# Kernel tuning notes

Measured on AMD Instinct MI355X. Metric: run time of the kernel, lower is better.

The kernel has to match this reference:

```python
import jax, jax.numpy as jnp
import numpy as np

N_NODES = 50000
N_EDGES = 800000
IN_CH = 128
OUT_CH = 64  # hidden = 2*OUT_CH = 128


def setup_inputs() -> dict:
    key = jax.random.key(0)
    ks = jax.random.split(key, 5)
    x = jax.random.normal(ks[0], (N_NODES, IN_CH), dtype=jnp.float32)
    edge_index = jax.random.randint(ks[1], (2, N_EDGES), 0, N_NODES, dtype=jnp.int32)
    # Glorot-ish scaled weights for the two GCNConv layers
    W1 = jax.random.normal(ks[2], (IN_CH, 2 * OUT_CH), dtype=jnp.float32) * 0.05
    b1 = jnp.zeros((2 * OUT_CH,), dtype=jnp.float32)
    W2 = jax.random.normal(ks[3], (2 * OUT_CH, OUT_CH), dtype=jnp.float32) * 0.05
    b2 = jnp.zeros((OUT_CH,), dtype=jnp.float32)
    return {"x": x, "edge_index": edge_index, "W1": W1, "b1": b1, "W2": W2, "b2": b2}


def reference(x, edge_index, W1, b1, W2, b2):
    N = x.shape[0]
    # GCN normalization with self-loops (PyG GCNConv default):
    # A_hat = A + I, deg from target nodes, norm = d_i^-1/2 * d_j^-1/2
    loops = jnp.arange(N, dtype=edge_index.dtype)
    row = jnp.concatenate([edge_index[0], loops])  # source
    col = jnp.concatenate([edge_index[1], loops])  # target
    deg = jax.ops.segment_sum(jnp.ones(row.shape, x.dtype), col, num_segments=N)
    dinv = jnp.where(deg > 0, jax.lax.rsqrt(deg), 0.0)
    norm = dinv[row] * dinv[col]  # [E+N]

    def conv(h, W, b):
        h = h @ W                           # [N, D_out] transform first (D_out <= D_in path)
        msg = norm[:, None] * h[row]        # gather + scale: [E+N, D_out]
        agg = jax.ops.segment_sum(msg, col, num_segments=N)
        return agg + b

    h = jax.nn.relu(conv(x, W1, b1))
    return conv(h, W2, b2)
```

## Files before the change

kernel.cpp:

```cpp
#include <hip/hip_runtime.h>
#include <hip/hip_bf16.h>
#include <hip/hip_fp16.h>

#define IN_CH  128
#define HID    128
#define OUTC   64

#define NSCAT 256
#define SLOTC 64
#define CAPB  6144
#define CAP2  6144

typedef _Float16 half8 __attribute__((ext_vector_type(8)));
typedef float float4v __attribute__((ext_vector_type(4)));

__global__ __launch_bounds__(256) void scatA_kernel(
        const int* __restrict__ src, const int* __restrict__ dst,
        unsigned* __restrict__ tmp2, ushort* __restrict__ cnts,
        const float* __restrict__ W1, const float* __restrict__ W2,
        _Float16* __restrict__ Wt1, _Float16* __restrict__ Wt2,
        int E, int N, int NBK, int chunk) {
    __shared__ int cnt[256];
    int t = threadIdx.x, blk = blockIdx.x;
    cnt[t] = 0;
    __syncthreads();
    int base = blk * chunk;
    int end = base + chunk; if (end > E) end = E;
    for (int e = base + t; e < end; e += 256) {
        unsigned d = (unsigned)dst[e];
        unsigned s = (unsigned)src[e];
        int b = d >> 8;
        int pos = atomicAdd(&cnt[b], 1);
        if (pos < SLOTC)
            tmp2[((size_t)(b << 8) + blk) * SLOTC + pos] = (d << 16) | s;
    }
    __syncthreads();
    if (t < NBK) {
        int c = cnt[t]; if (c > SLOTC) c = SLOTC;
        cnts[t * 256 + blk] = (ushort)c;
    }

    for (int idx = blk * 256 + t; idx < 128 * 128 + 128 * 64; idx += NSCAT * 256) {
        if (idx < 128 * 128) {
            int k = idx >> 7, nn = idx & 127;
            Wt1[nn * 128 + k] = (_Float16)W1[idx];
        } else {
            int j = idx - 128 * 128;
            int k = j >> 6, nn = j & 63;
            Wt2[nn * 128 + k] = (_Float16)W2[j];
        }
    }
}

__global__ __launch_bounds__(256) void csrB_kernel(
        const unsigned* __restrict__ tmp2, const ushort* __restrict__ cnts,
        int* __restrict__ off, ushort* __restrict__ degs, float* __restrict__ dinv,
        ushort* __restrict__ srcs,
        const float* __restrict__ x, _Float16* __restrict__ xh,
        int N, int NBK) {
    __shared__ int ex[257];
    __shared__ int h[256], cur[256];
    __shared__ unsigned ein[CAP2];
    __shared__ ushort outb[CAP2];
    __shared__ float dsh[256];
    int b = blockIdx.x, t = threadIdx.x;

    int c = cnts[b * 256 + t];
    h[t] = c;
    __syncthreads();
    for (int d = 1; d < 256; d <<= 1) {
        int v = (t >= d) ? h[t - d] : 0;
        __syncthreads();
        h[t] += v;
        __syncthreads();
    }
    ex[t] = h[t] - c;
    if (t == 255) ex[256] = h[255];
    __syncthreads();
    int total = ex[256]; if (total > CAP2) total = CAP2;

    for (int i = t; i < total; i += 256) {
        int lo = 0, hi = 255;
        while (lo < hi) {
            int mid = (lo + hi + 1) >> 1;
            if (ex[mid] <= i) lo = mid; else hi = mid - 1;
        }
        ein[i] = tmp2[((size_t)(b << 8) + lo) * SLOTC + (i - ex[lo])];
    }
    __syncthreads();

    h[t] = 0;
    __syncthreads();
    for (int i = t; i < total; i += 256)
        atomicAdd(&h[(ein[i] >> 16) & 255], 1);
    __syncthreads();
    int cdeg = h[t];
    for (int d = 1; d < 256; d <<= 1) {
        int v = (t >= d) ? h[t - d] : 0;
        __syncthreads();
        h[t] += v;
        __syncthreads();
    }
    int excl = h[t] - cdeg;
    int node = (b << 8) + t;
    float dv = rsqrtf((float)(cdeg + 1));
    if (node < N) {
        off[node] = b * CAPB + excl;
        degs[node] = (ushort)cdeg;
        dinv[node] = dv;
    }
    dsh[t] = (node < N) ? dv : 0.f;
    cur[t] = excl;
    __syncthreads();
    for (int i = t; i < total; i += 256) {
        unsigned v = ein[i];
        int pos = atomicAdd(&cur[(v >> 16) & 255], 1);
        outb[pos] = (ushort)(v & 0xFFFFu);
    }
    __syncthreads();
    for (int i = t; i < total; i += 256) srcs[b * CAPB + i] = outb[i];

    int rowbase = b << 8;
    for (int m = t; m < 256 * 16; m += 256) {
        int r = m >> 4, k = m & 15;
        int nd = rowbase + r;
        if (nd < N) {
            const float4* xp = (const float4*)(x + (size_t)nd * 128 + k * 8);
            float4 v0 = xp[0], v1 = xp[1];
            float di = dsh[r];
            half8 o = { (_Float16)(di * v0.x), (_Float16)(di * v0.y),
                        (_Float16)(di * v0.z), (_Float16)(di * v0.w),
                        (_Float16)(di * v1.x), (_Float16)(di * v1.y),
                        (_Float16)(di * v1.z), (_Float16)(di * v1.w) };
            ((half8*)xh)[(size_t)nd * 16 + k] = o;
        }
    }
}

__global__ __launch_bounds__(256) void agg1_kernel(const _Float16* __restrict__ xh,
                                                   const int* __restrict__ off,
                                                   const ushort* __restrict__ degs,
                                                   const ushort* __restrict__ srcs,
                                                   const float* __restrict__ dinv,
                                                   _Float16* __restrict__ A1, int N) {
    int grp = threadIdx.x >> 4;
    int p   = threadIdx.x & 15;
    int node = blockIdx.x * 16 + grp;
    if (node >= N) return;
    int s = off[node];
    int e = s + degs[node];

    const half8* xs = (const half8*)xh;
    float acc[8];
#pragma unroll
    for (int i = 0; i < 8; ++i) acc[i] = 0.f;

    int j = s;
    for (; j + 8 <= e; j += 8) {
        int i0 = srcs[j], i1 = srcs[j+1], i2 = srcs[j+2], i3 = srcs[j+3];
        int i4 = srcs[j+4], i5 = srcs[j+5], i6 = srcs[j+6], i7 = srcs[j+7];
        half8 u0 = xs[(size_t)i0 * 16 + p];
        half8 u1 = xs[(size_t)i1 * 16 + p];
        half8 u2 = xs[(size_t)i2 * 16 + p];
        half8 u3 = xs[(size_t)i3 * 16 + p];
        half8 u4 = xs[(size_t)i4 * 16 + p];
        half8 u5 = xs[(size_t)i5 * 16 + p];
        half8 u6 = xs[(size_t)i6 * 16 + p];
        half8 u7 = xs[(size_t)i7 * 16 + p];
#pragma unroll
        for (int i = 0; i < 8; ++i)
            acc[i] += ((float)u0[i] + (float)u1[i]) + ((float)u2[i] + (float)u3[i])
                    + ((float)u4[i] + (float)u5[i]) + ((float)u6[i] + (float)u7[i]);
    }
    if (j + 4 <= e) {
        int i0 = srcs[j], i1 = srcs[j+1], i2 = srcs[j+2], i3 = srcs[j+3];
        half8 u0 = xs[(size_t)i0 * 16 + p];
        half8 u1 = xs[(size_t)i1 * 16 + p];
        half8 u2 = xs[(size_t)i2 * 16 + p];
        half8 u3 = xs[(size_t)i3 * 16 + p];
#pragma unroll
        for (int i = 0; i < 8; ++i)
            acc[i] += ((float)u0[i] + (float)u1[i]) + ((float)u2[i] + (float)u3[i]);
        j += 4;
    }
    int r = e - j;
    if (r > 0) {
        int i0 = srcs[j];
        int i1 = srcs[r > 1 ? j + 1 : j];
        int i2 = srcs[r > 2 ? j + 2 : j];
        float w1 = (r > 1) ? 1.f : 0.f;
        float w2 = (r > 2) ? 1.f : 0.f;
        half8 u0 = xs[(size_t)i0 * 16 + p];
        half8 u1 = xs[(size_t)i1 * 16 + p];
        half8 u2 = xs[(size_t)i2 * 16 + p];
#pragma unroll
        for (int i = 0; i < 8; ++i)
            acc[i] += (float)u0[i] + w1 * (float)u1[i] + w2 * (float)u2[i];
    }

    float di = dinv[node];
    half8 sv = xs[(size_t)node * 16 + p];
    half8 hh;
#pragma unroll
    for (int i = 0; i < 8; ++i)
        hh[i] = (_Float16)(di * (acc[i] + (float)sv[i]));
    *((half8*)(A1 + (size_t)node * 128) + p) = hh;
}

#define TSTRIDE 140
__global__ __launch_bounds__(256) void gemm_fused_kernel(
        const _Float16* __restrict__ A1, const _Float16* __restrict__ Wt1,
        const float* __restrict__ b1, const _Float16* __restrict__ Wt2,
        const float* __restrict__ dinv, _Float16* __restrict__ H3s, int N) {
    __shared__ _Float16 tile[4][32 * TSTRIDE];
    int wave = threadIdx.x >> 6;
    int lane = threadIdx.x & 63;
    int n16 = lane & 15;
    int q   = lane >> 4;
    int rowBase = blockIdx.x * 128 + wave * 32;

    half8 a[2][4];
#pragma unroll
    for (int rt = 0; rt < 2; ++rt) {
        int row = rowBase + rt * 16 + n16;
        if (row >= N) row = N - 1;
        const _Float16* ap = A1 + (size_t)row * 128 + q * 8;
#pragma unroll
        for (int kb = 0; kb < 4; ++kb)
            a[rt][kb] = *(const half8*)(ap + kb * 32);
    }

    float4v acc1[2][8];
#pragma unroll
    for (int rt = 0; rt < 2; ++rt)
#pragma unroll
        for (int ct = 0; ct < 8; ++ct) acc1[rt][ct] = (float4v)0.f;
#pragma unroll
    for (int ct = 0; ct < 8; ++ct) {
        const _Float16* bp = Wt1 + (size_t)(ct * 16 + n16) * 128 + q * 8;
        half8 b[4];
#pragma unroll
        for (int kb = 0; kb < 4; ++kb) b[kb] = *(const half8*)(bp + kb * 32);
#pragma unroll
        for (int kb = 0; kb < 4; ++kb) {
            acc1[0][ct] = __builtin_amdgcn_mfma_f32_16x16x32_f16(a[0][kb], b[kb], acc1[0][ct], 0, 0, 0);
            acc1[1][ct] = __builtin_amdgcn_mfma_f32_16x16x32_f16(a[1][kb], b[kb], acc1[1][ct], 0, 0, 0);
        }
    }

    _Float16* tw = &tile[wave][0];
#pragma unroll
    for (int ct = 0; ct < 8; ++ct) {
        int col = ct * 16 + n16;
        float bv = b1[col];
#pragma unroll
        for (int rt = 0; rt < 2; ++rt)
#pragma unroll
            for (int r = 0; r < 4; ++r) {
                int row = rt * 16 + q * 4 + r;
                tw[row * TSTRIDE + col] = (_Float16)fmaxf(acc1[rt][ct][r] + bv, 0.f);
            }
    }
    __syncthreads();

    half8 a2[2][4];
#pragma unroll
    for (int rt = 0; rt < 2; ++rt) {
        const _Float16* tp = tw + (rt * 16 + n16) * TSTRIDE + q * 8;
#pragma unroll
        for (int kb = 0; kb < 4; ++kb)
            a2[rt][kb] = *(const half8*)(tp + kb * 32);
    }

    float4v acc2[2][4];
#pragma unroll
    for (int rt = 0; rt < 2; ++rt)
#pragma unroll
        for (int ct = 0; ct < 4; ++ct) acc2[rt][ct] = (float4v)0.f;
#pragma unroll
    for (int ct = 0; ct < 4; ++ct) {
        const _Float16* bp = Wt2 + (size_t)(ct * 16 + n16) * 128 + q * 8;
        half8 b[4];
#pragma unroll
        for (int kb = 0; kb < 4; ++kb) b[kb] = *(const half8*)(bp + kb * 32);
#pragma unroll
        for (int kb = 0; kb < 4; ++kb) {
            acc2[0][ct] = __builtin_amdgcn_mfma_f32_16x16x32_f16(a2[0][kb], b[kb], acc2[0][ct], 0, 0, 0);
            acc2[1][ct] = __builtin_amdgcn_mfma_f32_16x16x32_f16(a2[1][kb], b[kb], acc2[1][ct], 0, 0, 0);
        }
    }

#pragma unroll
    for (int rt = 0; rt < 2; ++rt)
#pragma unroll
        for (int ct = 0; ct < 4; ++ct) {
            int col = ct * 16 + n16;
#pragma unroll
            for (int r = 0; r < 4; ++r) {
                int row = rowBase + rt * 16 + q * 4 + r;
                if (row < N)
                    H3s[(size_t)row * OUTC + col] = (_Float16)(acc2[rt][ct][r] * dinv[row]);
            }
        }
}

__global__ __launch_bounds__(256) void agg2_kernel(const _Float16* __restrict__ H3s,
                                                   const int* __restrict__ off,
                                                   const ushort* __restrict__ degs,
                                                   const ushort* __restrict__ srcs,
                                                   const float* __restrict__ dinv,
                                                   const float* __restrict__ bias,
                                                   float* __restrict__ out, int N) {
    int grp = threadIdx.x >> 3;
    int p   = threadIdx.x & 7;
    int node = blockIdx.x * 32 + grp;
    if (node >= N) return;
    int s = off[node];
    int e = s + degs[node];

    const half8* hs = (const half8*)H3s;
    float acc[8];
#pragma unroll
    for (int i = 0; i < 8; ++i) acc[i] = 0.f;

    int j = s;
    for (; j + 8 <= e; j += 8) {
        int i0 = srcs[j], i1 = srcs[j+1], i2 = srcs[j+2], i3 = srcs[j+3];
        int i4 = srcs[j+4], i5 = srcs[j+5], i6 = srcs[j+6], i7 = srcs[j+7];
        half8 u0 = hs[(size_t)i0 * 8 + p];
        half8 u1 = hs[(size_t)i1 * 8 + p];
        half8 u2 = hs[(size_t)i2 * 8 + p];
        half8 u3 = hs[(size_t)i3 * 8 + p];
        half8 u4 = hs[(size_t)i4 * 8 + p];
        half8 u5 = hs[(size_t)i5 * 8 + p];
        half8 u6 = hs[(size_t)i6 * 8 + p];
        half8 u7 = hs[(size_t)i7 * 8 + p];
#pragma unroll
        for (int i = 0; i < 8; ++i)
            acc[i] += ((float)u0[i] + (float)u1[i]) + ((float)u2[i] + (float)u3[i])
                    + ((float)u4[i] + (float)u5[i]) + ((float)u6[i] + (float)u7[i]);
    }
    if (j + 4 <= e) {
        int i0 = srcs[j], i1 = srcs[j+1], i2 = srcs[j+2], i3 = srcs[j+3];
        half8 u0 = hs[(size_t)i0 * 8 + p];
        half8 u1 = hs[(size_t)i1 * 8 + p];
        half8 u2 = hs[(size_t)i2 * 8 + p];
        half8 u3 = hs[(size_t)i3 * 8 + p];
#pragma unroll
        for (int i = 0; i < 8; ++i)
            acc[i] += ((float)u0[i] + (float)u1[i]) + ((float)u2[i] + (float)u3[i]);
        j += 4;
    }
    int r = e - j;
    if (r > 0) {
        int i0 = srcs[j];
        int i1 = srcs[r > 1 ? j + 1 : j];
        int i2 = srcs[r > 2 ? j + 2 : j];
        float w1 = (r > 1) ? 1.f : 0.f;
        float w2 = (r > 2) ? 1.f : 0.f;
        half8 u0 = hs[(size_t)i0 * 8 + p];
        half8 u1 = hs[(size_t)i1 * 8 + p];
        half8 u2 = hs[(size_t)i2 * 8 + p];
#pragma unroll
        for (int i = 0; i < 8; ++i)
            acc[i] += (float)u0[i] + w1 * (float)u1[i] + w2 * (float)u2[i];
    }

    float di = dinv[node];
    half8 sv = hs[(size_t)node * 8 + p];
    const float4* bp = (const float4*)(bias + p * 8);
    float4 b0 = bp[0], b1 = bp[1];
    float4 o0, o1;
    o0.x = di * (acc[0] + (float)sv[0]) + b0.x;
    o0.y = di * (acc[1] + (float)sv[1]) + b0.y;
    o0.z = di * (acc[2] + (float)sv[2]) + b0.z;
    o0.w = di * (acc[3] + (float)sv[3]) + b0.w;
    o1.x = di * (acc[4] + (float)sv[4]) + b1.x;
    o1.y = di * (acc[5] + (float)sv[5]) + b1.y;
    o1.z = di * (acc[6] + (float)sv[6]) + b1.z;
    o1.w = di * (acc[7] + (float)sv[7]) + b1.w;
    float4* op = (float4*)(out + (size_t)node * 64 + p * 8);
    op[0] = o0; op[1] = o1;
}

extern "C" void kernel_launch(void* const* d_in, const int* in_sizes, int n_in,
                              void* d_out, int out_size, void* d_ws, size_t ws_size,
                              hipStream_t stream) {
    const float* x   = (const float*)d_in[0];
    const int*   ei  = (const int*)d_in[1];
    const float* W1  = (const float*)d_in[2];
    const float* b1  = (const float*)d_in[3];
    const float* W2  = (const float*)d_in[4];
    const float* b2  = (const float*)d_in[5];
    float* out = (float*)d_out;

    const int N = in_sizes[0] / IN_CH;
    const int E = in_sizes[1] / 2;
    const int* src = ei;
    const int* dst = ei + E;

    const int NBK = (N + 255) >> 8;
    const int chunk = (E + NSCAT - 1) / NSCAT;

    auto align256 = [](size_t v) { return (v + 255) & ~(size_t)255; };
    char* w = (char*)d_ws;
    int* off = (int*)w;              w += align256((size_t)N * 4);
    ushort* degs = (ushort*)w;       w += align256((size_t)N * 2);
    float* dinv = (float*)w;         w += align256((size_t)N * 4);
    ushort* cnts = (ushort*)w;       w += align256((size_t)NBK * 256 * 2);
    ushort* srcs = (ushort*)w;       w += align256((size_t)NBK * CAPB * 2);
    _Float16* Wt1 = (_Float16*)w;    w += align256((size_t)HID * 128 * 2);
    _Float16* Wt2 = (_Float16*)w;    w += align256((size_t)OUTC * 128 * 2);
    size_t reg1 = align256((size_t)NBK * 256 * SLOTC * 4);
    if (reg1 < align256((size_t)N * HID * 2)) reg1 = align256((size_t)N * HID * 2);
    unsigned* tmp2 = (unsigned*)w;
    _Float16* A1 = (_Float16*)w;     w += reg1;
    _Float16* xh = (_Float16*)w;
    _Float16* H3s = (_Float16*)w;    w += align256((size_t)N * HID * 2);

    scatA_kernel<<<NSCAT, 256, 0, stream>>>(src, dst, tmp2, cnts,
                                            W1, W2, Wt1, Wt2, E, N, NBK, chunk);
    csrB_kernel<<<NBK, 256, 0, stream>>>(tmp2, cnts, off, degs, dinv, srcs,
                                         x, xh, N, NBK);

    agg1_kernel<<<(N + 15) / 16, 256, 0, stream>>>(xh, off, degs, srcs, dinv, A1, N);
    gemm_fused_kernel<<<(N + 127) / 128, 256, 0, stream>>>(A1, Wt1, b1, Wt2, dinv, H3s, N);
    agg2_kernel<<<(N + 31) / 32, 256, 0, stream>>>(H3s, off, degs, srcs, dinv, b2, out, N);
}
```

Measured before the change: 184.0 us.

## Fuse layer-1 aggregation into the GEMM kernel via shared-memory tile

New measurement: 189.1 us. 2.7% more time.

```diff
diff --git a/kernel.cpp b/kernel.cpp
--- a/kernel.cpp
+++ b/kernel.cpp
@@ -10,9 +10,24 @@
 #define SLOTC 64
 #define CAPB  6144
 #define CAP2  6144
+#define TSTRIDE 140
 
 typedef _Float16 half8 __attribute__((ext_vector_type(8)));
+typedef _Float16 half4v __attribute__((ext_vector_type(4)));
 typedef float float4v __attribute__((ext_vector_type(4)));
+
+__device__ __forceinline__ void vacc(float4v& a0, float4v& a1, half8 u) {
+    half4v lo = __builtin_shufflevector(u, u, 0, 1, 2, 3);
+    half4v hi = __builtin_shufflevector(u, u, 4, 5, 6, 7);
+    a0 += __builtin_convertvector(lo, float4v);
+    a1 += __builtin_convertvector(hi, float4v);
+}
+__device__ __forceinline__ void vaccw(float4v& a0, float4v& a1, half8 u, float w) {
+    half4v lo = __builtin_shufflevector(u, u, 0, 1, 2, 3);
+    half4v hi = __builtin_shufflevector(u, u, 4, 5, 6, 7);
+    a0 += w * __builtin_convertvector(lo, float4v);
+    a1 += w * __builtin_convertvector(hi, float4v);
+}
 
 __global__ __launch_bounds__(256) void scatA_kernel(
         const int* __restrict__ src, const int* __restrict__ dst,
@@ -137,94 +152,95 @@
     }
 }
 
-__global__ __launch_bounds__(256) void agg1_kernel(const _Float16* __restrict__ xh,
-                                                   const int* __restrict__ off,
-                                                   const ushort* __restrict__ degs,
-                                                   const ushort* __restrict__ srcs,
-                                                   const float* __restrict__ dinv,
-                                                   _Float16* __restrict__ A1, int N) {
-    int grp = threadIdx.x >> 4;
-    int p   = threadIdx.x & 15;
-    int node = blockIdx.x * 16 + grp;
-    if (node >= N) return;
-    int s = off[node];
-    int e = s + degs[node];
-
+__global__ __launch_bounds__(256) void agg1gemm_kernel(
+        const _Float16* __restrict__ xh,
+        const int* __restrict__ off, const ushort* __restrict__ degs,
+        const ushort* __restrict__ srcs, const float* __restrict__ dinv,
+        const _Float16* __restrict__ Wt1, const float* __restrict__ b1,
+        const _Float16* __restrict__ Wt2, _Float16* __restrict__ H3s, int N) {
+    __shared__ _Float16 tile[4][32 * TSTRIDE];
+    int t = threadIdx.x;
+    int grp = t >> 4, p = t & 15;
+    int base = blockIdx.x * 128;
     const half8* xs = (const half8*)xh;
-    float acc[8];
-#pragma unroll
-    for (int i = 0; i < 8; ++i) acc[i] = 0.f;
-
-    int j = s;
-    for (; j + 8 <= e; j += 8) {
-        int i0 = srcs[j], i1 = srcs[j+1], i2 = srcs[j+2], i3 = srcs[j+3];
-        int i4 = srcs[j+4], i5 = srcs[j+5], i6 = srcs[j+6], i7 = srcs[j+7];
-        half8 u0 = xs[(size_t)i0 * 16 + p];
-        half8 u1 = xs[(size_t)i1 * 16 + p];
-        half8 u2 = xs[(size_t)i2 * 16 + p];
-        half8 u3 = xs[(size_t)i3 * 16 + p];
-        half8 u4 = xs[(size_t)i4 * 16 + p];
-        half8 u5 = xs[(size_t)i5 * 16 + p];
-        half8 u6 = xs[(size_t)i6 * 16 + p];
-        half8 u7 = xs[(size_t)i7 * 16 + p];
-#pragma unroll
-        for (int i = 0; i < 8; ++i)
-            acc[i] += ((float)u0[i] + (float)u1[i]) + ((float)u2[i] + (float)u3[i])
-                    + ((float)u4[i] + (float)u5[i]) + ((float)u6[i] + (float)u7[i]);
-    }
-    if (j + 4 <= e) {
-        int i0 = srcs[j], i1 = srcs[j+1], i2 = srcs[j+2], i3 = srcs[j+3];
-        half8 u0 = xs[(size_t)i0 * 16 + p];
-        half8 u1 = xs[(size_t)i1 * 16 + p];
-        half8 u2 = xs[(size_t)i2 * 16 + p];
-        half8 u3 = xs[(size_t)i3 * 16 + p];
-#pragma unroll
-        for (int i = 0; i < 8; ++i)
-            acc[i] += ((float)u0[i] + (float)u1[i]) + ((float)u2[i] + (float)u3[i]);
-        j += 4;
-    }
-    int r = e - j;
-    if (r > 0) {
-        int i0 = srcs[j];
-        int i1 = srcs[r > 1 ? j + 1 : j];
-        int i2 = srcs[r > 2 ? j + 2 : j];
-        float w1 = (r > 1) ? 1.f : 0.f;
-        float w2 = (r > 2) ? 1.f : 0.f;
-        half8 u0 = xs[(size_t)i0 * 16 + p];
-        half8 u1 = xs[(size_t)i1 * 16 + p];
-        half8 u2 = xs[(size_t)i2 * 16 + p];
-#pragma unroll
-        for (int i = 0; i < 8; ++i)
-            acc[i] += (float)u0[i] + w1 * (float)u1[i] + w2 * (float)u2[i];
-    }
-
-    float di = dinv[node];
-    half8 sv = xs[(size_t)node * 16 + p];
-    half8 hh;
-#pragma unroll
-    for (int i = 0; i < 8; ++i)
-        hh[i] = (_Float16)(di * (acc[i] + (float)sv[i]));
-    *((half8*)(A1 + (size_t)node * 128) + p) = hh;
-}
-
-#define TSTRIDE 140
-__global__ __launch_bounds__(256) void gemm_fused_kernel(
-        const _Float16* __restrict__ A1, const _Float16* __restrict__ Wt1,
-        const float* __restrict__ b1, const _Float16* __restrict__ Wt2,
-        const float* __restrict__ dinv, _Float16* __restrict__ H3s, int N) {
-    __shared__ _Float16 tile[4][32 * TSTRIDE];
-    int wave = threadIdx.x >> 6;
-    int lane = threadIdx.x & 63;
+
+    for (int it = 0; it < 8; ++it) {
+        int r = grp * 8 + it;
+        int node = base + r;
+        if (node < N) {
+            int s = off[node];
+            int e = s + degs[node];
+            float4v a0 = (float4v)0.f, a1 = (float4v)0.f;
+            float4v c0 = (float4v)0.f, c1 = (float4v)0.f;
+            int j = s;
+            for (; j + 8 <= e; j += 8) {
+                int i0 = srcs[j], i1 = srcs[j+1], i2 = srcs[j+2], i3 = srcs[j+3];
+                int i4 = srcs[j+4], i5 = srcs[j+5], i6 = srcs[j+6], i7 = srcs[j+7];
+                half8 u0 = xs[(size_t)i0 * 16 + p];
+                half8 u1 = xs[(size_t)i1 * 16 + p];
+                half8 u2 = xs[(size_t)i2 * 16 + p];
+                half8 u3 = xs[(size_t)i3 * 16 + p];
+                half8 u4 = xs[(size_t)i4 * 16 + p];
+                half8 u5 = xs[(size_t)i5 * 16 + p];
+                half8 u6 = xs[(size_t)i6 * 16 + p];
+                half8 u7 = xs[(size_t)i7 * 16 + p];
+                vacc(a0, a1, u0); vacc(c0, c1, u1);
+                vacc(a0, a1, u2); vacc(c0, c1, u3);
+                vacc(a0, a1, u4); vacc(c0, c1, u5);
+                vacc(a0, a1, u6); vacc(c0, c1, u7);
+            }
+            if (j + 4 <= e) {
+                int i0 = srcs[j], i1 = srcs[j+1], i2 = srcs[j+2], i3 = srcs[j+3];
+                half8 u0 = xs[(size_t)i0 * 16 + p];
+                half8 u1 = xs[(size_t)i1 * 16 + p];
+                half8 u2 = xs[(size_t)i2 * 16 + p];
+                half8 u3 = xs[(size_t)i3 * 16 + p];
+                vacc(a0, a1, u0); vacc(c0, c1, u1);
+                vacc(a0, a1, u2); vacc(c0, c1, u3);
+                j += 4;
+            }
+            int rm = e - j;
+            if (rm > 0) {
+                int i0 = srcs[j];
+                int i1 = srcs[rm > 1 ? j + 1 : j];
+                int i2 = srcs[rm > 2 ? j + 2 : j];
+                float w1 = (rm > 1) ? 1.f : 0.f;
+                float w2 = (rm > 2) ? 1.f : 0.f;
+                half8 u0 = xs[(size_t)i0 * 16 + p];
+                half8 u1 = xs[(size_t)i1 * 16 + p];
+                half8 u2 = xs[(size_t)i2 * 16 + p];
+                vacc(a0, a1, u0);
+                vaccw(c0, c1, u1, w1);
+                vaccw(c0, c1, u2, w2);
+            }
+            a0 += c0; a1 += c1;
+            half8 sv = xs[(size_t)node * 16 + p];
+            half4v slo = __builtin_shufflevector(sv, sv, 0, 1, 2, 3);
+            half4v shi = __builtin_shufflevector(sv, sv, 4, 5, 6, 7);
+            a0 += __builtin_convertvector(slo, float4v);
+            a1 += __builtin_convertvector(shi, float4v);
+            float di = dinv[node];
+            a0 *= di; a1 *= di;
+            half4v h0 = __builtin_convertvector(a0, half4v);
+            half4v h1 = __builtin_convertvector(a1, half4v);
+            _Float16* twp = &tile[r >> 5][(r & 31) * TSTRIDE + p * 8];
+            *(half4v*)twp = h0;
+            *(half4v*)(twp + 4) = h1;
+        }
+    }
+    __syncthreads();
+
+    int wave = t >> 6;
+    int lane = t & 63;
     int n16 = lane & 15;
     int q   = lane >> 4;
-    int rowBase = blockIdx.x * 128 + wave * 32;
+    int rowBase = base + wave * 32;
+    _Float16* tw = &tile[wave][0];
 
     half8 a[2][4];
 #pragma unroll
     for (int rt = 0; rt < 2; ++rt) {
-        int row = rowBase + rt * 16 + n16;
-        if (row >= N) row = N - 1;
-        const _Float16* ap = A1 + (size_t)row * 128 + q * 8;
+        const _Float16* ap = tw + (rt * 16 + n16) * TSTRIDE + q * 8;
 #pragma unroll
         for (int kb = 0; kb < 4; ++kb)
             a[rt][kb] = *(const half8*)(ap + kb * 32);
@@ -248,7 +264,6 @@
         }
     }
 
-    _Float16* tw = &tile[wave][0];
 #pragma unroll
     for (int ct = 0; ct < 8; ++ct) {
         int col = ct * 16 + n16;
@@ -319,9 +334,8 @@
     int e = s + degs[node];
 
     const half8* hs = (const half8*)H3s;
-    float acc[8];
-#pragma unroll
-    for (int i = 0; i < 8; ++i) acc[i] = 0.f;
+    float4v a0 = (float4v)0.f, a1 = (float4v)0.f;
+    float4v c0 = (float4v)0.f, c1 = (float4v)0.f;
 
     int j = s;
     for (; j + 8 <= e; j += 8) {
@@ -335,10 +349,10 @@
         half8 u5 = hs[(size_t)i5 * 8 + p];
         half8 u6 = hs[(size_t)i6 * 8 + p];
         half8 u7 = hs[(size_t)i7 * 8 + p];
-#pragma unroll
-        for (int i = 0; i < 8; ++i)
-            acc[i] += ((float)u0[i] + (float)u1[i]) + ((float)u2[i] + (float)u3[i])
-                    + ((float)u4[i] + (float)u5[i]) + ((float)u6[i] + (float)u7[i]);
+        vacc(a0, a1, u0); vacc(c0, c1, u1);
+        vacc(a0, a1, u2); vacc(c0, c1, u3);
+        vacc(a0, a1, u4); vacc(c0, c1, u5);
+        vacc(a0, a1, u6); vacc(c0, c1, u7);
     }
     if (j + 4 <= e) {
         int i0 = srcs[j], i1 = srcs[j+1], i2 = srcs[j+2], i3 = srcs[j+3];
@@ -346,40 +360,36 @@
         half8 u1 = hs[(size_t)i1 * 8 + p];
         half8 u2 = hs[(size_t)i2 * 8 + p];
         half8 u3 = hs[(size_t)i3 * 8 + p];
-#pragma unroll
-        for (int i = 0; i < 8; ++i)
-            acc[i] += ((float)u0[i] + (float)u1[i]) + ((float)u2[i] + (float)u3[i]);
+        vacc(a0, a1, u0); vacc(c0, c1, u1);
+        vacc(a0, a1, u2); vacc(c0, c1, u3);
         j += 4;
     }
-    int r = e - j;
-    if (r > 0) {
+    int rm = e - j;
+    if (rm > 0) {
         int i0 = srcs[j];
-        int i1 = srcs[r > 1 ? j + 1 : j];
-        int i2 = srcs[r > 2 ? j + 2 : j];
-        float w1 = (r > 1) ? 1.f : 0.f;
-        float w2 = (r > 2) ? 1.f : 0.f;
+        int i1 = srcs[rm > 1 ? j + 1 : j];
+        int i2 = srcs[rm > 2 ? j + 2 : j];
+        float w1 = (rm > 1) ? 1.f : 0.f;
+        float w2 = (rm > 2) ? 1.f : 0.f;
         half8 u0 = hs[(size_t)i0 * 8 + p];
         half8 u1 = hs[(size_t)i1 * 8 + p];
         half8 u2 = hs[(size_t)i2 * 8 + p];
-#pragma unroll
-        for (int i = 0; i < 8; ++i)
-            acc[i] += (float)u0[i] + w1 * (float)u1[i] + w2 * (float)u2[i];
-    }
+        vacc(a0, a1, u0);
+        vaccw(c0, c1, u1, w1);
+        vaccw(c0, c1, u2, w2);
+    }
+    a0 += c0; a1 += c1;
 
     float di = dinv[node];
     half8 sv = hs[(size_t)node * 8 + p];
-    const float4* bp = (const float4*)(bias + p * 8);
-    float4 b0 = bp[0], b1 = bp[1];
-    float4 o0, o1;
-    o0.x = di * (acc[0] + (float)sv[0]) + b0.x;
-    o0.y = di * (acc[1] + (float)sv[1]) + b0.y;
-    o0.z = di * (acc[2] + (float)sv[2]) + b0.z;
-    o0.w = di * (acc[3] + (float)sv[3]) + b0.w;
-    o1.x = di * (acc[4] + (float)sv[4]) + b1.x;
-    o1.y = di * (acc[5] + (float)sv[5]) + b1.y;
-    o1.z = di * (acc[6] + (float)sv[6]) + b1.z;
-    o1.w = di * (acc[7] + (float)sv[7]) + b1.w;
-    float4* op = (float4*)(out + (size_t)node * 64 + p * 8);
+    half4v slo = __builtin_shufflevector(sv, sv, 0, 1, 2, 3);
+    half4v shi = __builtin_shufflevector(sv, sv, 4, 5, 6, 7);
+    a0 += __builtin_convertvector(slo, float4v);
+    a1 += __builtin_convertvector(shi, float4v);
+    const float4v* bp = (const float4v*)(bias + p * 8);
+    float4v o0 = di * a0 + bp[0];
+    float4v o1 = di * a1 + bp[1];
+    float4v* op = (float4v*)(out + (size_t)node * 64 + p * 8);
     op[0] = o0; op[1] = o1;
 }
 
@@ -412,18 +422,16 @@
     _Float16* Wt1 = (_Float16*)w;    w += align256((size_t)HID * 128 * 2);
     _Float16* Wt2 = (_Float16*)w;    w += align256((size_t)OUTC * 128 * 2);
     size_t reg1 = align256((size_t)NBK * 256 * SLOTC * 4);
-    if (reg1 < align256((size_t)N * HID * 2)) reg1 = align256((size_t)N * HID * 2);
     unsigned* tmp2 = (unsigned*)w;
-    _Float16* A1 = (_Float16*)w;     w += reg1;
-    _Float16* xh = (_Float16*)w;
-    _Float16* H3s = (_Float16*)w;    w += align256((size_t)N * HID * 2);
+    _Float16* H3s = (_Float16*)w;    w += reg1;
+    _Float16* xh = (_Float16*)w;     w += align256((size_t)N * HID * 2);
 
     scatA_kernel<<<NSCAT, 256, 0, stream>>>(src, dst, tmp2, cnts,
                                             W1, W2, Wt1, Wt2, E, N, NBK, chunk);
     csrB_kernel<<<NBK, 256, 0, stream>>>(tmp2, cnts, off, degs, dinv, srcs,
                                          x, xh, N, NBK);
 
-    agg1_kernel<<<(N + 15) / 16, 256, 0, stream>>>(xh, off, degs, srcs, dinv, A1, N);
-    gemm_fused_kernel<<<(N + 127) / 128, 256, 0, stream>>>(A1, Wt1, b1, Wt2, dinv, H3s, N);
+    agg1gemm_kernel<<<(N + 127) / 128, 256, 0, stream>>>(xh, off, degs, srcs, dinv,
+                                                         Wt1, b1, Wt2, H3s, N);
     agg2_kernel<<<(N + 31) / 32, 256, 0, stream>>>(H3s, off, degs, srcs, dinv, b2, out, N);
 }
```
